# Optimization experiments

Hardware: AMD Instinct MI355X
Metric: run time of the kernel (lower is better)

The kernel has to match this reference:

```python
import jax, jax.numpy as jnp
import numpy as np

# graph sizes: G graphs of N_PER nodes each (block-diagonal batched graph)
G, N_PER, F, NHID, E_PER = 128, 512, 128, 128, 4096
N = G * N_PER
E = G * E_PER
L1, L2, L3 = 4, 2, 2            # PANConv filter sizes (conv1 uses init filter_size=4)
K1, K2, K3 = N_PER // 2, N_PER // 4, N_PER // 8  # ratio=0.5 top-k per pooling stage


def setup_inputs() -> dict:
    ks = jax.random.split(jax.random.key(0), 10)
    rng = np.random.default_rng(0)
    off = (np.arange(G) * N_PER)[:, None]
    src = (rng.integers(0, N_PER, size=(G, E_PER)) + off).reshape(-1)
    dst = (rng.integers(0, N_PER, size=(G, E_PER)) + off).reshape(-1)
    edge_index = jnp.asarray(np.stack([src, dst]).astype(np.int32))
    batch = jnp.repeat(jnp.arange(G, dtype=jnp.int32), N_PER)
    def w(k, shp, fan):
        return jax.random.normal(k, shp, jnp.float32) / np.float32(np.sqrt(fan))
    z = lambda *s: jnp.zeros(s, jnp.float32)
    return dict(
        x=jax.random.normal(ks[0], (N, F), jnp.float32),
        edge_index=edge_index, batch=batch,
        lump_W=w(ks[1], (F, NHID), F), lump_b=z(NHID),
        conv1_W=w(ks[2], (NHID, NHID), NHID), conv1_b=z(NHID),
        conv2_W=w(ks[3], (NHID, NHID), NHID), conv2_b=z(NHID),
        conv3_W=w(ks[4], (NHID, NHID), NHID), conv3_b=z(NHID),
        pool1_p=w(ks[5], (NHID,), NHID), pool1_beta=jnp.full((2,), 0.5, jnp.float32),
        pool2_p=w(ks[6], (NHID,), NHID), pool2_beta=jnp.full((2,), 0.5, jnp.float32),
        pool3_p=w(ks[7], (NHID,), NHID), pool3_beta=jnp.full((2,), 0.5, jnp.float32),
        lin1_W=w(ks[8], (NHID, NHID // 2), NHID), lin1_b=z(NHID // 2),
        lin2_W=w(ks[9], (NHID // 2, 1), NHID // 2), lin2_b=z(1),
    )


def _pan_prop(h, src, dst, ew, L):
    # (sum_{l=0..L} A^l) @ h, A weighted by edge weights ew, via iterated gather/scatter
    acc, y = h, h
    n = h.shape[0]
    for _ in range(L):
        y = jax.ops.segment_sum(y[src] * ew[:, None], dst, num_segments=n)
        acc = acc + y
    return acc


def _pan_conv(x, src, dst, ew, W, b, L):
    # PANConv: M = Z^{-1/2} (sum_{l<=L} A^l) Z^{-1/2};  out = M x W + b
    d = _pan_prop(jnp.ones((x.shape[0], 1), x.dtype), src, dst, ew, L)[:, 0]
    dinv = jax.lax.rsqrt(jnp.maximum(d, 1e-12))
    h = dinv[:, None] * _pan_prop(dinv[:, None] * x, src, dst, ew, L)
    return h @ W + b


def _pan_pool(x, src, dst, ew, p, beta, n_per, k):
    # PANPooling: score = beta0*(x.p)/||p|| + beta1*node_strength; per-graph top-k
    n = x.shape[0]
    deg = jax.ops.segment_sum(ew, dst, num_segments=n)
    score = beta[0] * (x @ p) / jnp.linalg.norm(p) + beta[1] * deg
    _, idx = jax.lax.top_k(score.reshape(G, n_per), k)          # [G, k] local indices
    perm = (idx + (jnp.arange(G) * n_per)[:, None]).reshape(-1)  # [G*k] global
    x_new = x[perm] * jnp.tanh(score[perm])[:, None]
    inv = jnp.zeros((n,), jnp.int32).at[perm].set(jnp.arange(G * k, dtype=jnp.int32))
    mask = jnp.zeros((n,), x.dtype).at[perm].set(1.0)
    # keep edge arrays fixed-size: dropped edges get weight 0 (same math as filtering)
    return x_new, inv[src], inv[dst], ew * mask[src] * mask[dst], perm


def reference(x, edge_index, batch, lump_W, lump_b, conv1_W, conv1_b, conv2_W, conv2_b,
              conv3_W, conv3_b, pool1_p, pool1_beta, pool2_p, pool2_beta, pool3_p,
              pool3_beta, lin1_W, lin1_b, lin2_W, lin2_b):
    src, dst = edge_index[0], edge_index[1]
    ew = jnp.ones((src.shape[0],), x.dtype)
    h = x @ lump_W + lump_b                                   # PANLump lift
    h = _pan_conv(h, src, dst, ew, conv1_W, conv1_b, L1)
    h, src, dst, ew, perm1 = _pan_pool(h, src, dst, ew, pool1_p, pool1_beta, N_PER, K1)
    h = _pan_conv(h, src, dst, ew, conv2_W, conv2_b, L2)
    h, src, dst, ew, perm2 = _pan_pool(h, src, dst, ew, pool2_p, pool2_beta, K1, K2)
    h = _pan_conv(h, src, dst, ew, conv3_W, conv3_b, L3)
    h, src, dst, ew, perm3 = _pan_pool(h, src, dst, ew, pool3_p, pool3_beta, K2, K3)
    seg = jnp.repeat(jnp.arange(G, dtype=jnp.int32), K3)
    mean = jax.ops.segment_sum(h, seg, num_segments=G) / jnp.float32(K3)  # scatter_mean
    out = jax.nn.relu(mean @ lin1_W + lin1_b) @ lin2_W + lin2_b           # [G, 1]
    return out
```

## Files before the change

kernel.cpp:

```cpp
#include <hip/hip_runtime.h>
#include <math.h>

#define G_     128
#define E_     524288
#define EPG    4096
#define DEGMAX 48

typedef __attribute__((ext_vector_type(8))) short bf16x8;
typedef __attribute__((ext_vector_type(4))) float f32x4;
typedef __attribute__((ext_vector_type(4))) unsigned short u16x4;

__device__ inline void split_bf16(float x, short& hi, short& lo){
    unsigned u = __float_as_uint(x);
    hi = (short)(u >> 16);
    float hf = __uint_as_float(u & 0xffff0000u);
    unsigned r = __float_as_uint(x - hf);
    lo = (short)(r >> 16);
}

template<int WAVES>
__device__ void gemm_body(char* smem, int bid, const float* __restrict__ X,
        const float* __restrict__ W, const float* __restrict__ bias, float* __restrict__ Y,
        const float* __restrict__ p, const float* __restrict__ beta,
        const int* __restrict__ cntv, float* __restrict__ score){
    short* wsh = (short*)smem;
    short* wsl = (short*)(smem + 34816);
    float* bsh = (float*)(smem + 69632);
    float* qs  = (float*)(smem + 70144);
    float* rednorm = (float*)(smem + 70656);
    const int NT = WAVES*64;
    int t = threadIdx.x;
    for (int e = t; e < 16384; e += NT){
        int k = e >> 7, n = e & 127;
        short hi, lo; split_bf16(W[e], hi, lo);
        wsh[n*136 + k] = hi; wsl[n*136 + k] = lo;
    }
    if (t < 128) bsh[t] = bias[t];
    if (score && t < 64){ float a = p[t], b = p[t+64]; rednorm[t] = a*a + b*b; }
    __syncthreads();
    float b1 = 0.f;
    if (score){
        if (t == 0){ float s = 0.f; for (int i = 0; i < 64; i++) s += rednorm[i]; rednorm[0] = sqrtf(s); }
        __syncthreads();
        if (t < 128) qs[t] = beta[0] * p[t] / rednorm[0];
        b1 = beta[1];
        __syncthreads();
    }
    int wave = t >> 6, lane = t & 63;
    int ln = lane & 15, q = lane >> 4;
    size_t rb = (size_t)bid * (WAVES*16);
    const float* xrow = &X[(rb + wave*16 + ln)*128 + q*8];
    f32x4 acc[8];
    #pragma unroll
    for (int i = 0; i < 8; i++) acc[i] = (f32x4){0.f,0.f,0.f,0.f};
    #pragma unroll
    for (int kc = 0; kc < 4; kc++){
        float4 xa = *(const float4*)(xrow + kc*32);
        float4 xb = *(const float4*)(xrow + kc*32 + 4);
        bf16x8 ah, al; short hi, lo;
        split_bf16(xa.x, hi, lo); ah[0]=hi; al[0]=lo;
        split_bf16(xa.y, hi, lo); ah[1]=hi; al[1]=lo;
        split_bf16(xa.z, hi, lo); ah[2]=hi; al[2]=lo;
        split_bf16(xa.w, hi, lo); ah[3]=hi; al[3]=lo;
        split_bf16(xb.x, hi, lo); ah[4]=hi; al[4]=lo;
        split_bf16(xb.y, hi, lo); ah[5]=hi; al[5]=lo;
        split_bf16(xb.z, hi, lo); ah[6]=hi; al[6]=lo;
        split_bf16(xb.w, hi, lo); ah[7]=hi; al[7]=lo;
        #pragma unroll
        for (int nt = 0; nt < 8; nt++){
            int wo = (nt*16 + ln)*136 + kc*32 + q*8;
            bf16x8 bh = *(const bf16x8*)&wsh[wo];
            bf16x8 bl = *(const bf16x8*)&wsl[wo];
            acc[nt] = __builtin_amdgcn_mfma_f32_16x16x32_bf16(ah, bh, acc[nt], 0, 0, 0);
            acc[nt] = __builtin_amdgcn_mfma_f32_16x16x32_bf16(ah, bl, acc[nt], 0, 0, 0);
            acc[nt] = __builtin_amdgcn_mfma_f32_16x16x32_bf16(al, bh, acc[nt], 0, 0, 0);
        }
    }
    #pragma unroll
    for (int nt = 0; nt < 8; nt++){
        int c = nt*16 + ln;
        float bb = bsh[c];
        #pragma unroll
        for (int r = 0; r < 4; r++){
            Y[(rb + wave*16 + q*4 + r)*128 + c] = acc[nt][r] + bb;
        }
    }
    if (score){
        #pragma unroll
        for (int r = 0; r < 4; r++){
            float sp = 0.f;
            #pragma unroll
            for (int nt = 0; nt < 8; nt++){
                int c = nt*16 + ln;
                sp += (acc[nt][r] + bsh[c]) * qs[c];
            }
            sp += __shfl_xor(sp, 1);
            sp += __shfl_xor(sp, 2);
            sp += __shfl_xor(sp, 4);
            sp += __shfl_xor(sp, 8);
            if (ln == 0){
                int row = (int)rb + wave*16 + q*4 + r;
                score[row] = sp + b1 * (float)cntv[row];
            }
        }
    }
}

__device__ void prep1_body(char* smem, int g, const int* __restrict__ ei,
        int* __restrict__ cnt, unsigned short* __restrict__ csrcp,
        int* __restrict__ permg, float* __restrict__ dinvg){
    int*   lcnt  = (int*)smem;
    float* y     = (float*)(smem + 2048);
    int*   bins  = (int*)(smem + 6144);
    int*   permS = (int*)(smem + 6400);
    int t = threadIdx.x, gbase = g*512;
    lcnt[t] = 0;
    if (t < 64) bins[t] = 0;
    __syncthreads();
    for (int i = t; i < EPG; i += 512){
        int e = g*EPG + i;
        int sv = ei[e] & 511;
        int d  = ei[E_ + e] & 511;
        int slot = atomicAdd(&lcnt[d], 1);
        if (slot < DEGMAX) csrcp[(size_t)(gbase + d)*DEGMAX + slot] = (unsigned short)sv;
    }
    __syncthreads();
    int rawc = lcnt[t];
    cnt[gbase + t] = rawc;
    int dc = min(rawc, DEGMAX);
    {
        int e4 = (dc + 3) & ~3;
        for (int s2 = dc; s2 < e4; s2++) csrcp[(size_t)(gbase + t)*DEGMAX + s2] = 0;
    }
    atomicAdd(&bins[dc], 1);
    __syncthreads();
    if (t < 64){
        int v0 = bins[t], s = v0;
        #pragma unroll
        for (int off = 1; off < 64; off <<= 1){
            int n = __shfl_up(s, off);
            if (t >= off) s += n;
        }
        bins[t] = s - v0;
    }
    __syncthreads();
    {
        int slot = atomicAdd(&bins[dc], 1);
        int pk = t | (dc << 16);
        permS[slot] = pk;
        permg[gbase + slot] = pk;
    }
    __syncthreads();
    int pk = permS[t];
    int pv = pk & 0xffff, pd = pk >> 16;
    y[pv] = 1.f;
    __syncthreads();
    float dacc = 1.f;
    int cur = 0;
    for (int l = 0; l < 4; l++){
        const float* la = &y[cur*512];
        float s = 0.f;
        int nq = (pd + 3) >> 2;
        const u16x4* cp = (const u16x4*)(csrcp + (size_t)(gbase + pv)*DEGMAX);
        u16x4 oc = cp[0];
        #pragma unroll 1
        for (int jq = 0; jq < nq; jq++){
            u16x4 ocn = cp[jq + 1];
            s += (la[(int)oc[0]] + la[(int)oc[1]]) + (la[(int)oc[2]] + la[(int)oc[3]]);
            oc = ocn;
        }
        if (nq) s -= (float)(nq*4 - pd) * la[0];
        y[(1^cur)*512 + pv] = s;
        dacc += s;
        __syncthreads();
        cur ^= 1;
    }
    dinvg[gbase + pv] = rsqrtf(fmaxf(dacc, 1e-12f));
}

__global__ __launch_bounds__(512) void k_lump_prep(const float* __restrict__ x,
        const float* __restrict__ lumpW, const float* __restrict__ lumpb, float* __restrict__ A,
        const int* __restrict__ ei, int* __restrict__ cnt, unsigned short* __restrict__ csr1,
        int* __restrict__ perm1, float* __restrict__ dinv1){
    __shared__ __align__(16) char smem[70912];
    if (blockIdx.x < G_) prep1_body(smem, blockIdx.x, ei, cnt, csr1, perm1, dinv1);
    else gemm_body<8>(smem, blockIdx.x - G_, x, lumpW, lumpb, A,
                      nullptr, nullptr, nullptr, nullptr);
}

template<int WAVES>
__global__ __launch_bounds__(WAVES*64) void k_gemm_mfma(const float* __restrict__ X,
        const float* __restrict__ W, const float* __restrict__ bias, float* __restrict__ Y,
        const float* __restrict__ p, const float* __restrict__ beta,
        const int* __restrict__ cntv, float* __restrict__ score){
    __shared__ __align__(16) char smem[70912];
    gemm_body<WAVES>(smem, blockIdx.x, X, W, bias, Y, p, beta, cntv, score);
}

template<int NPER, int L, int IT, bool SEL>
__global__ __launch_bounds__(1024)
void k_prop(const int* __restrict__ permg, const float* __restrict__ dinvg,
        const unsigned short* __restrict__ csrcp,
        const float* __restrict__ X, const int* __restrict__ selg,
        const float* __restrict__ thg, float* __restrict__ OUT){
    constexpr int QMAX = (EPG + 3*NPER)/4 + 4;
    constexpr int NW   = NPER/64;
    __shared__ __align__(16) float y[NPER*32];
    __shared__ float dinvs[NPER];
    __shared__ u16x4 csrl[QMAX];
    __shared__ unsigned short qoffS[NPER];
    __shared__ int wsumS[NW];
    int g = blockIdx.x, fq = blockIdx.y, gbase = g*NPER;
    int t = threadIdx.x;
    int f4 = (t & 7)*4;
    int fo = fq*32 + f4;
    if (t < NPER) dinvs[t] = dinvg[gbase + t];
    int pkr[IT];
    {
        int wv = t >> 6, gi = (t >> 3) & 7;
        #pragma unroll
        for (int it = 0; it < IT; it++){
            int ch = (it & 1) ? (15 - wv) : wv;
            pkr[it] = permg[gbase + (16*it + ch)*8 + gi];
        }
    }
    int nqv = 0, pvv = 0;
    if (t < NPER){
        int pk2 = permg[gbase + t];
        pvv = pk2 & 0xffff;
        nqv = ((pk2 >> 16) + 3) >> 2;
    }
    int incl = nqv;
    #pragma unroll
    for (int off2 = 1; off2 < 64; off2 <<= 1){
        int n2 = __shfl_up(incl, off2);
        if ((t & 63) >= off2) incl += n2;
    }
    if (t < NPER && (t & 63) == 63) wsumS[t >> 6] = incl;
    __syncthreads();
    if (t == 0){
        int run = 0;
        #pragma unroll
        for (int w = 0; w < NW; w++){ int v2 = wsumS[w]; wsumS[w] = run; run += v2; }
    }
    __syncthreads();
    if (t < NPER){
        int qo = incl - nqv + wsumS[t >> 6];
        qoffS[pvv] = (unsigned short)qo;
        const u16x4* gp = (const u16x4*)(csrcp + (size_t)(gbase + pvv)*DEGMAX);
        for (int j = 0; j < nqv; j++) csrl[qo + j] = gp[j];
    }
    float4 acc[IT];
    #pragma unroll
    for (int it = 0; it < IT; it++){
        int v = pkr[it] & 0xffff;
        float d = dinvs[v];
        size_t row;
        if (SEL){
            row = (size_t)selg[gbase + v];
            d *= thg[gbase + v];
        } else {
            row = (size_t)(gbase + v);
        }
        float4 w = *(const float4*)&X[row*128 + fo];
        w.x*=d; w.y*=d; w.z*=d; w.w*=d;
        acc[it] = w;
        *(float4*)&y[v*32 + f4] = w;
    }
    __syncthreads();
    for (int l = 0; l < L; l++){
        float4 s[IT];
        #pragma unroll
        for (int it = 0; it < IT; it++){
            int pk = pkr[it];
            int v = pk & 0xffff;
            int c = pk >> 16;
            int nq = (c + 3) >> 2;
            const u16x4* cp = &csrl[(int)qoffS[v]];
            float4 ss = make_float4(0.f,0.f,0.f,0.f);
            u16x4 oc = cp[0];
            #pragma unroll 1
            for (int jq = 0; jq < nq; jq++){
                u16x4 ocn = cp[jq + 1];
                float4 w0 = *(const float4*)&y[((int)oc[0])*32 + f4];
                float4 w1 = *(const float4*)&y[((int)oc[1])*32 + f4];
                float4 w2 = *(const float4*)&y[((int)oc[2])*32 + f4];
                float4 w3 = *(const float4*)&y[((int)oc[3])*32 + f4];
                ss.x += (w0.x + w1.x) + (w2.x + w3.x);
                ss.y += (w0.y + w1.y) + (w2.y + w3.y);
                ss.z += (w0.z + w1.z) + (w2.z + w3.z);
                ss.w += (w0.w + w1.w) + (w2.w + w3.w);
                oc = ocn;
            }
            if (nq){
                float fp = (float)(nq*4 - c);
                float4 z = *(const float4*)&y[f4];
                ss.x -= fp*z.x; ss.y -= fp*z.y; ss.z -= fp*z.z; ss.w -= fp*z.w;
            }
            s[it] = ss;
        }
        __syncthreads();
        #pragma unroll
        for (int it = 0; it < IT; it++){
            int v = pkr[it] & 0xffff;
            *(float4*)&y[v*32 + f4] = s[it];
            acc[it].x+=s[it].x; acc[it].y+=s[it].y; acc[it].z+=s[it].z; acc[it].w+=s[it].w;
        }
        __syncthreads();
    }
    #pragma unroll
    for (int it = 0; it < IT; it++){
        int v = pkr[it] & 0xffff;
        float d = dinvs[v];
        float4 w = acc[it];
        w.x*=d; w.y*=d; w.z*=d; w.w*=d;
        *(float4*)&OUT[(size_t)(gbase + v)*128 + fo] = w;
    }
}

template<int NPER, bool BUILD>
__global__ __launch_bounds__(512) void k_pooltop(const float* __restrict__ score_in,
        const int* __restrict__ esrc_in, const int* __restrict__ edst_in,
        int* __restrict__ esrc_out, int* __restrict__ edst_out,
        int* __restrict__ cnt_next, unsigned short* __restrict__ csrcp,
        int* __restrict__ permg, float* __restrict__ dinvg,
        int* __restrict__ selg, float* __restrict__ thg){
    __shared__ __align__(16) float sc[NPER];
    __shared__ int  nid[NPER];
    __shared__ int  lcnt[NPER/2];
    __shared__ int  bins[64];
    __shared__ int  permS[NPER/2];
    const int K = NPER/2;
    int g = blockIdx.x, t = threadIdx.x, gbase = g*NPER;
    if (t < K) lcnt[t] = 0;
    if (t < 64) bins[t] = 0;
    if (t < NPER) sc[t] = score_in[gbase + t];
    __syncthreads();
    if (t < NPER){
        float s = sc[t];
        int rank = 0;
        const float4* sc4 = (const float4*)sc;
        #pragma unroll 8
        for (int j4 = 0; j4 < NPER/4; j4++){
            float4 v = sc4[j4];
            int j = j4*4;
            rank += (v.x > s) || (v.x == s && (j+0) < t);
            rank += (v.y > s) || (v.y == s && (j+1) < t);
            rank += (v.z > s) || (v.z == s && (j+2) < t);
            rank += (v.w > s) || (v.w == s && (j+3) < t);
        }
        if (rank < K){
            nid[t] = g*K + rank;
            selg[g*K + rank] = gbase + t;
            thg[g*K + rank]  = tanhf(s);
        } else nid[t] = -1;
    }
    __syncthreads();
    if (BUILD){
        for (int i = t; i < EPG; i += 512){
            int e = g*EPG + i;
            int d = edst_in[e];
            if (d < 0) continue;
            int s_ = esrc_in[e];
            int ns = nid[s_ - gbase], nd = nid[d - gbase];
            if ((ns | nd) < 0){ edst_out[e] = -1; }
            else {
                esrc_out[e] = ns; edst_out[e] = nd;
                int slot = atomicAdd(&lcnt[nd & (K-1)], 1);
                if (slot < DEGMAX) csrcp[(size_t)nd*DEGMAX + slot] = (unsigned short)(ns & (K-1));
            }
        }
        __syncthreads();
        float* yd = sc;
        int rawc = 0, dc = 0;
        if (t < K){
            rawc = lcnt[t];
            cnt_next[g*K + t] = rawc;
            dc = min(rawc, DEGMAX);
            int e4 = (dc + 3) & ~3;
            for (int s2 = dc; s2 < e4; s2++) csrcp[(size_t)(g*K + t)*DEGMAX + s2] = 0;
            atomicAdd(&bins[dc], 1);
        }
        __syncthreads();
        if (t < 64){
            int v0 = bins[t], s = v0;
            #pragma unroll
            for (int off = 1; off < 64; off <<= 1){
                int n = __shfl_up(s, off);
                if (t >= off) s += n;
            }
            bins[t] = s - v0;
        }
        __syncthreads();
        if (t < K){
            int slot = atomicAdd(&bins[dc], 1);
            permS[slot] = t | (dc << 16);
            permg[g*K + slot] = permS[slot];
        }
        __syncthreads();
        int pv = 0, pd = 0;
        if (t < K){
            int pk = permS[t];
            pv = pk & 0xffff; pd = pk >> 16;
            yd[pv] = 1.f;
        }
        __syncthreads();
        float dacc = 1.f;
        int cur = 0;
        for (int l = 0; l < 2; l++){
            if (t < K){
                const float* la = &yd[cur*K];
                float s = 0.f;
                int nq = (pd + 3) >> 2;
                const u16x4* cp = (const u16x4*)(csrcp + (size_t)(g*K + pv)*DEGMAX);
                u16x4 oc = cp[0];
                #pragma unroll 1
                for (int jq = 0; jq < nq; jq++){
                    u16x4 ocn = cp[jq + 1];
                    s += (la[(int)oc[0]] + la[(int)oc[1]]) + (la[(int)oc[2]] + la[(int)oc[3]]);
                    oc = ocn;
                }
                if (nq) s -= (float)(nq*4 - pd) * la[0];
                yd[(1^cur)*K + pv] = s;
                dacc += s;
            }
            __syncthreads();
            cur ^= 1;
        }
        if (t < K) dinvg[g*K + pv] = rsqrtf(fmaxf(dacc, 1e-12f));
    }
}

__global__ __launch_bounds__(512) void k_stage3(const float* __restrict__ X,
        const float* __restrict__ W, const float* __restrict__ bias,
        const float* __restrict__ p, const float* __restrict__ beta,
        const int* __restrict__ cntv,
        const float* __restrict__ W1, const float* __restrict__ b1,
        const float* __restrict__ W2, const float* __restrict__ b2,
        float* __restrict__ out){
    __shared__ __align__(16) char smem[70912];
    __shared__ float scs[128];
    __shared__ float thS[64];
    __shared__ int   selS[64];
    __shared__ float mr[128];
    short* wsh = (short*)smem;
    short* wsl = (short*)(smem + 34816);
    float* bsh = (float*)(smem + 69632);
    float* qs  = (float*)(smem + 70144);
    float* rednorm = (float*)(smem + 70656);
    int g = blockIdx.x, t = threadIdx.x;
    for (int e = t; e < 16384; e += 512){
        int k = e >> 7, n = e & 127;
        short hi, lo; split_bf16(W[e], hi, lo);
        wsh[n*136 + k] = hi; wsl[n*136 + k] = lo;
    }
    if (t < 128) bsh[t] = bias[t];
    if (t < 64){ float a = p[t], b = p[t+64]; rednorm[t] = a*a + b*b; }
    __syncthreads();
    if (t == 0){ float s = 0.f; for (int i = 0; i < 64; i++) s += rednorm[i]; rednorm[0] = sqrtf(s); }
    __syncthreads();
    if (t < 128) qs[t] = beta[0] * p[t] / rednorm[0];
    float b1v = beta[1];
    __syncthreads();
    int wave = t >> 6, lane = t & 63;
    int ln = lane & 15, q = lane >> 4;
    const float* xrow = &X[((size_t)g*128 + wave*16 + ln)*128 + q*8];
    f32x4 acc[8];
    #pragma unroll
    for (int i = 0; i < 8; i++) acc[i] = (f32x4){0.f,0.f,0.f,0.f};
    #pragma unroll
    for (int kc = 0; kc < 4; kc++){
        float4 xa = *(const float4*)(xrow + kc*32);
        float4 xb = *(const float4*)(xrow + kc*32 + 4);
        bf16x8 ah, al; short hi, lo;
        split_bf16(xa.x, hi, lo); ah[0]=hi; al[0]=lo;
        split_bf16(xa.y, hi, lo); ah[1]=hi; al[1]=lo;
        split_bf16(xa.z, hi, lo); ah[2]=hi; al[2]=lo;
        split_bf16(xa.w, hi, lo); ah[3]=hi; al[3]=lo;
        split_bf16(xb.x, hi, lo); ah[4]=hi; al[4]=lo;
        split_bf16(xb.y, hi, lo); ah[5]=hi; al[5]=lo;
        split_bf16(xb.z, hi, lo); ah[6]=hi; al[6]=lo;
        split_bf16(xb.w, hi, lo); ah[7]=hi; al[7]=lo;
        #pragma unroll
        for (int nt = 0; nt < 8; nt++){
            int wo = (nt*16 + ln)*136 + kc*32 + q*8;
            bf16x8 bh = *(const bf16x8*)&wsh[wo];
            bf16x8 bl = *(const bf16x8*)&wsl[wo];
            acc[nt] = __builtin_amdgcn_mfma_f32_16x16x32_bf16(ah, bh, acc[nt], 0, 0, 0);
            acc[nt] = __builtin_amdgcn_mfma_f32_16x16x32_bf16(ah, bl, acc[nt], 0, 0, 0);
            acc[nt] = __builtin_amdgcn_mfma_f32_16x16x32_bf16(al, bh, acc[nt], 0, 0, 0);
        }
    }
    #pragma unroll
    for (int r = 0; r < 4; r++){
        float sp = 0.f;
        #pragma unroll
        for (int nt = 0; nt < 8; nt++){
            int c = nt*16 + ln;
            sp += (acc[nt][r] + bsh[c]) * qs[c];
        }
        sp += __shfl_xor(sp, 1);
        sp += __shfl_xor(sp, 2);
        sp += __shfl_xor(sp, 4);
        sp += __shfl_xor(sp, 8);
        if (ln == 0){
            int rl = wave*16 + q*4 + r;
            scs[rl] = sp + b1v * (float)cntv[g*128 + rl];
        }
    }
    __syncthreads();
    float* Yl = (float*)smem;
    #pragma unroll
    for (int nt = 0; nt < 8; nt++){
        int c = nt*16 + ln;
        float bb = bsh[c];
        #pragma unroll
        for (int r = 0; r < 4; r++){
            Yl[(wave*16 + q*4 + r)*132 + c] = acc[nt][r] + bb;
        }
    }
    __syncthreads();
    if (t < 128){
        float s = scs[t];
        int rank = 0;
        const float4* sc4 = (const float4*)scs;
        #pragma unroll 8
        for (int j4 = 0; j4 < 32; j4++){
            float4 v = sc4[j4];
            int j = j4*4;
            rank += (v.x > s) || (v.x == s && (j+0) < t);
            rank += (v.y > s) || (v.y == s && (j+1) < t);
            rank += (v.z > s) || (v.z == s && (j+2) < t);
            rank += (v.w > s) || (v.w == s && (j+3) < t);
        }
        if (rank < 64){ selS[rank] = t; thS[rank] = tanhf(s); }
    }
    __syncthreads();
    if (t < 128){
        float s = 0.f;
        #pragma unroll 8
        for (int r = 0; r < 64; r++) s += Yl[selS[r]*132 + t] * thS[r];
        mr[t] = s * (1.f/64.f);
    }
    __syncthreads();
    if (t < 64){
        float a = b1[t];
        #pragma unroll 8
        for (int k = 0; k < 128; k++) a += mr[k]*W1[k*64 + t];
        a = fmaxf(a, 0.f);
        float r = a * W2[t];
        #pragma unroll
        for (int off = 32; off > 0; off >>= 1) r += __shfl_down(r, off);
        if (t == 0) out[g] = r + b2[0];
    }
}

extern "C" void kernel_launch(void* const* d_in, const int* in_sizes, int n_in,
                              void* d_out, int out_size, void* d_ws, size_t ws_size,
                              hipStream_t stream){
    (void)in_sizes; (void)n_in; (void)out_size; (void)ws_size;
    const float* x     = (const float*)d_in[0];
    const int*   ei    = (const int*)d_in[1];
    const float* lumpW = (const float*)d_in[3];
    const float* lumpb = (const float*)d_in[4];
    const float* convW[3]    = {(const float*)d_in[5], (const float*)d_in[7], (const float*)d_in[9]};
    const float* convB[3]    = {(const float*)d_in[6], (const float*)d_in[8], (const float*)d_in[10]};
    const float* poolP[3]    = {(const float*)d_in[11], (const float*)d_in[13], (const float*)d_in[15]};
    const float* poolBeta[3] = {(const float*)d_in[12], (const float*)d_in[14], (const float*)d_in[16]};
    const float* lin1W = (const float*)d_in[17];
    const float* lin1b = (const float*)d_in[18];
    const float* lin2W = (const float*)d_in[19];
    const float* lin2b = (const float*)d_in[20];
    float* out = (float*)d_out;

    char* w8 = (char*)d_ws;
    size_t off = 0;
    auto alloc = [&](size_t bytes)->char*{
        char* p = w8 + off; off += (bytes + 255) & ~(size_t)255; return p;
    };
    float* A     = (float*)alloc((size_t)65536*128*4);
    float* Bb    = (float*)alloc((size_t)65536*128*4);
    int*   srcA  = (int*)alloc((size_t)E_*4);
    int*   dstA  = (int*)alloc((size_t)E_*4);
    unsigned short* csr1 = (unsigned short*)alloc((size_t)65536*DEGMAX*2);
    unsigned short* csr2 = (unsigned short*)alloc((size_t)32768*DEGMAX*2);
    unsigned short* csr3 = (unsigned short*)alloc((size_t)16384*DEGMAX*2);
    int*   cntA  = (int*)alloc((size_t)(65536+32768+16384)*4);
    int*   cnt1 = cntA, *cnt2 = cntA + 65536, *cnt3 = cntA + 98304;
    int*   perm1 = (int*)alloc((size_t)65536*4);
    int*   perm2 = (int*)alloc((size_t)32768*4);
    int*   perm3 = (int*)alloc((size_t)16384*4);
    float* dinv1 = (float*)alloc((size_t)65536*4);
    float* dinv2 = (float*)alloc((size_t)32768*4);
    float* dinv3 = (float*)alloc((size_t)16384*4);
    float* score1 = (float*)alloc((size_t)65536*4);
    float* score2 = (float*)alloc((size_t)32768*4);
    int*   sel2  = (int*)alloc((size_t)32768*4);
    int*   sel3  = (int*)alloc((size_t)16384*4);
    float* th2   = (float*)alloc((size_t)32768*4);
    float* th3   = (float*)alloc((size_t)16384*4);

    k_lump_prep<<<G_ + 512, 512, 0, stream>>>(x, lumpW, lumpb, A, ei, cnt1, csr1, perm1, dinv1);

    k_prop<512,4,4,false><<<dim3(G_,4), 1024, 0, stream>>>(perm1, dinv1, csr1, A,
            nullptr, nullptr, Bb);
    k_gemm_mfma<8><<<512, 512, 0, stream>>>(Bb, convW[0], convB[0], A,
            poolP[0], poolBeta[0], cnt1, score1);
    k_pooltop<512,true><<<G_, 512, 0, stream>>>(score1, ei, ei + E_, srcA, dstA,
            cnt2, csr2, perm2, dinv2, sel2, th2);

    k_prop<256,2,2,true><<<dim3(G_,4), 1024, 0, stream>>>(perm2, dinv2, csr2, A,
            sel2, th2, Bb);
    k_gemm_mfma<8><<<256, 512, 0, stream>>>(Bb, convW[1], convB[1], A,
            poolP[1], poolBeta[1], cnt2, score2);
    k_pooltop<256,true><<<G_, 512, 0, stream>>>(score2, srcA, dstA, srcA, dstA,
            cnt3, csr3, perm3, dinv3, sel3, th3);

    k_prop<128,2,1,true><<<dim3(G_,4), 1024, 0, stream>>>(perm3, dinv3, csr3, A,
            sel3, th3, Bb);
    k_stage3<<<G_, 512, 0, stream>>>(Bb, convW[2], convB[2],
            poolP[2], poolBeta[2], cnt3, lin1W, lin1b, lin2W, lin2b, out);
}
```

Baseline: 298.0 us.

## Build CSR in LDS in prep kernel and read CSR from global in prop

Result: faster. 276.9 us (-7.1%).

```diff
diff --git a/kernel.cpp b/kernel.cpp
--- a/kernel.cpp
+++ b/kernel.cpp
@@ -106,88 +106,6 @@
     }
 }
 
-__device__ void prep1_body(char* smem, int g, const int* __restrict__ ei,
-        int* __restrict__ cnt, unsigned short* __restrict__ csrcp,
-        int* __restrict__ permg, float* __restrict__ dinvg){
-    int*   lcnt  = (int*)smem;
-    float* y     = (float*)(smem + 2048);
-    int*   bins  = (int*)(smem + 6144);
-    int*   permS = (int*)(smem + 6400);
-    int t = threadIdx.x, gbase = g*512;
-    lcnt[t] = 0;
-    if (t < 64) bins[t] = 0;
-    __syncthreads();
-    for (int i = t; i < EPG; i += 512){
-        int e = g*EPG + i;
-        int sv = ei[e] & 511;
-        int d  = ei[E_ + e] & 511;
-        int slot = atomicAdd(&lcnt[d], 1);
-        if (slot < DEGMAX) csrcp[(size_t)(gbase + d)*DEGMAX + slot] = (unsigned short)sv;
-    }
-    __syncthreads();
-    int rawc = lcnt[t];
-    cnt[gbase + t] = rawc;
-    int dc = min(rawc, DEGMAX);
-    {
-        int e4 = (dc + 3) & ~3;
-        for (int s2 = dc; s2 < e4; s2++) csrcp[(size_t)(gbase + t)*DEGMAX + s2] = 0;
-    }
-    atomicAdd(&bins[dc], 1);
-    __syncthreads();
-    if (t < 64){
-        int v0 = bins[t], s = v0;
-        #pragma unroll
-        for (int off = 1; off < 64; off <<= 1){
-            int n = __shfl_up(s, off);
-            if (t >= off) s += n;
-        }
-        bins[t] = s - v0;
-    }
-    __syncthreads();
-    {
-        int slot = atomicAdd(&bins[dc], 1);
-        int pk = t | (dc << 16);
-        permS[slot] = pk;
-        permg[gbase + slot] = pk;
-    }
-    __syncthreads();
-    int pk = permS[t];
-    int pv = pk & 0xffff, pd = pk >> 16;
-    y[pv] = 1.f;
-    __syncthreads();
-    float dacc = 1.f;
-    int cur = 0;
-    for (int l = 0; l < 4; l++){
-        const float* la = &y[cur*512];
-        float s = 0.f;
-        int nq = (pd + 3) >> 2;
-        const u16x4* cp = (const u16x4*)(csrcp + (size_t)(gbase + pv)*DEGMAX);
-        u16x4 oc = cp[0];
-        #pragma unroll 1
-        for (int jq = 0; jq < nq; jq++){
-            u16x4 ocn = cp[jq + 1];
-            s += (la[(int)oc[0]] + la[(int)oc[1]]) + (la[(int)oc[2]] + la[(int)oc[3]]);
-            oc = ocn;
-        }
-        if (nq) s -= (float)(nq*4 - pd) * la[0];
-        y[(1^cur)*512 + pv] = s;
-        dacc += s;
-        __syncthreads();
-        cur ^= 1;
-    }
-    dinvg[gbase + pv] = rsqrtf(fmaxf(dacc, 1e-12f));
-}
-
-__global__ __launch_bounds__(512) void k_lump_prep(const float* __restrict__ x,
-        const float* __restrict__ lumpW, const float* __restrict__ lumpb, float* __restrict__ A,
-        const int* __restrict__ ei, int* __restrict__ cnt, unsigned short* __restrict__ csr1,
-        int* __restrict__ perm1, float* __restrict__ dinv1){
-    __shared__ __align__(16) char smem[70912];
-    if (blockIdx.x < G_) prep1_body(smem, blockIdx.x, ei, cnt, csr1, perm1, dinv1);
-    else gemm_body<8>(smem, blockIdx.x - G_, x, lumpW, lumpb, A,
-                      nullptr, nullptr, nullptr, nullptr);
-}
-
 template<int WAVES>
 __global__ __launch_bounds__(WAVES*64) void k_gemm_mfma(const float* __restrict__ X,
         const float* __restrict__ W, const float* __restrict__ bias, float* __restrict__ Y,
@@ -197,19 +115,89 @@
     gemm_body<WAVES>(smem, blockIdx.x, X, W, bias, Y, p, beta, cntv, score);
 }
 
+__global__ __launch_bounds__(512) void k_prep1(const int* __restrict__ ei,
+        int* __restrict__ cnt, unsigned short* __restrict__ csrcp,
+        int* __restrict__ permg, float* __restrict__ dinvg){
+    __shared__ int   lcnt[512];
+    __shared__ __align__(16) unsigned short csrS[512*DEGMAX + 8];
+    __shared__ float y[1024];
+    __shared__ int   bins[64];
+    __shared__ int   permS[512];
+    int g = blockIdx.x, t = threadIdx.x, gbase = g*512;
+    lcnt[t] = 0;
+    if (t < 64) bins[t] = 0;
+    unsigned* c32 = (unsigned*)csrS;
+    for (int i = t; i < 512*DEGMAX/2 + 4; i += 512) c32[i] = 0;
+    __syncthreads();
+    for (int i = t; i < EPG; i += 512){
+        int e = g*EPG + i;
+        int sv = ei[e] & 511;
+        int d  = ei[E_ + e] & 511;
+        int slot = atomicAdd(&lcnt[d], 1);
+        if (slot < DEGMAX) csrS[d*DEGMAX + slot] = (unsigned short)sv;
+    }
+    __syncthreads();
+    {
+        unsigned* dst = (unsigned*)(csrcp + (size_t)gbase*DEGMAX);
+        for (int i = t; i < 512*DEGMAX/2; i += 512) dst[i] = c32[i];
+    }
+    int rawc = lcnt[t];
+    cnt[gbase + t] = rawc;
+    int dc = min(rawc, DEGMAX);
+    atomicAdd(&bins[dc], 1);
+    __syncthreads();
+    if (t < 64){
+        int v0 = bins[t], s = v0;
+        #pragma unroll
+        for (int off = 1; off < 64; off <<= 1){
+            int n = __shfl_up(s, off);
+            if (t >= off) s += n;
+        }
+        bins[t] = s - v0;
+    }
+    __syncthreads();
+    {
+        int slot = atomicAdd(&bins[dc], 1);
+        int pk = t | (dc << 16);
+        permS[slot] = pk;
+        permg[gbase + slot] = pk;
+    }
+    __syncthreads();
+    int pk = permS[t];
+    int pv = pk & 0xffff, pd = pk >> 16;
+    y[pv] = 1.f;
+    __syncthreads();
+    float dacc = 1.f;
+    int cur = 0;
+    for (int l = 0; l < 4; l++){
+        const float* la = &y[cur*512];
+        float s = 0.f;
+        int nq = (pd + 3) >> 2;
+        const u16x4* cp = (const u16x4*)(csrS + pv*DEGMAX);
+        u16x4 oc = cp[0];
+        #pragma unroll 1
+        for (int jq = 0; jq < nq; jq++){
+            u16x4 ocn = cp[jq + 1];
+            s += (la[(int)oc[0]] + la[(int)oc[1]]) + (la[(int)oc[2]] + la[(int)oc[3]]);
+            oc = ocn;
+        }
+        if (nq) s -= (float)(nq*4 - pd) * la[0];
+        y[(1^cur)*512 + pv] = s;
+        dacc += s;
+        __syncthreads();
+        cur ^= 1;
+    }
+    dinvg[gbase + pv] = rsqrtf(fmaxf(dacc, 1e-12f));
+}
+
 template<int NPER, int L, int IT, bool SEL>
 __global__ __launch_bounds__(1024)
 void k_prop(const int* __restrict__ permg, const float* __restrict__ dinvg,
         const unsigned short* __restrict__ csrcp,
         const float* __restrict__ X, const int* __restrict__ selg,
         const float* __restrict__ thg, float* __restrict__ OUT){
-    constexpr int QMAX = (EPG + 3*NPER)/4 + 4;
-    constexpr int NW   = NPER/64;
     __shared__ __align__(16) float y[NPER*32];
     __shared__ float dinvs[NPER];
-    __shared__ u16x4 csrl[QMAX];
-    __shared__ unsigned short qoffS[NPER];
-    __shared__ int wsumS[NW];
     int g = blockIdx.x, fq = blockIdx.y, gbase = g*NPER;
     int t = threadIdx.x;
     int f4 = (t & 7)*4;
@@ -224,32 +212,7 @@
             pkr[it] = permg[gbase + (16*it + ch)*8 + gi];
         }
     }
-    int nqv = 0, pvv = 0;
-    if (t < NPER){
-        int pk2 = permg[gbase + t];
-        pvv = pk2 & 0xffff;
-        nqv = ((pk2 >> 16) + 3) >> 2;
-    }
-    int incl = nqv;
-    #pragma unroll
-    for (int off2 = 1; off2 < 64; off2 <<= 1){
-        int n2 = __shfl_up(incl, off2);
-        if ((t & 63) >= off2) incl += n2;
-    }
-    if (t < NPER && (t & 63) == 63) wsumS[t >> 6] = incl;
-    __syncthreads();
-    if (t == 0){
-        int run = 0;
-        #pragma unroll
-        for (int w = 0; w < NW; w++){ int v2 = wsumS[w]; wsumS[w] = run; run += v2; }
-    }
-    __syncthreads();
-    if (t < NPER){
-        int qo = incl - nqv + wsumS[t >> 6];
-        qoffS[pvv] = (unsigned short)qo;
-        const u16x4* gp = (const u16x4*)(csrcp + (size_t)(gbase + pvv)*DEGMAX);
-        for (int j = 0; j < nqv; j++) csrl[qo + j] = gp[j];
-    }
+    __syncthreads();
     float4 acc[IT];
     #pragma unroll
     for (int it = 0; it < IT; it++){
@@ -273,10 +236,9 @@
         #pragma unroll
         for (int it = 0; it < IT; it++){
             int pk = pkr[it];
-            int v = pk & 0xffff;
             int c = pk >> 16;
             int nq = (c + 3) >> 2;
-            const u16x4* cp = &csrl[(int)qoffS[v]];
+            const u16x4* cp = (const u16x4*)(csrcp + (size_t)(gbase + (pk & 0xffff))*DEGMAX);
             float4 ss = make_float4(0.f,0.f,0.f,0.f);
             u16x4 oc = cp[0];
             #pragma unroll 1
@@ -600,7 +562,9 @@
     float* th2   = (float*)alloc((size_t)32768*4);
     float* th3   = (float*)alloc((size_t)16384*4);
 
-    k_lump_prep<<<G_ + 512, 512, 0, stream>>>(x, lumpW, lumpb, A, ei, cnt1, csr1, perm1, dinv1);
+    k_prep1<<<G_, 512, 0, stream>>>(ei, cnt1, csr1, perm1, dinv1);
+    k_gemm_mfma<8><<<512, 512, 0, stream>>>(x, lumpW, lumpb, A,
+            nullptr, nullptr, nullptr, nullptr);
 
     k_prop<512,4,4,false><<<dim3(G_,4), 1024, 0, stream>>>(perm1, dinv1, csr1, A,
             nullptr, nullptr, Bb);
```
